# Kernel tuning notes

Hardware: AMD Instinct MI355X
Metric: run time of the kernel (lower is better)

The kernel has to match this reference:

```python
import jax, jax.numpy as jnp
import numpy as np

N = 10000   # nodes
E = 160000  # edges
D = 32      # hidden_dim == out_dim
IN = 2      # 'pos' node features
STEPS = 3   # GatedGraphConv n_steps


def setup_inputs() -> dict:
    key = jax.random.key(0)
    ks = jax.random.split(key, 16)
    s = 0.1  # init scale
    inp = {
        "x": jax.random.normal(ks[0], (N, IN), jnp.float32),
        "src": jax.random.randint(ks[1], (E,), 0, N, jnp.int64),
        "dst": jax.random.randint(ks[2], (E,), 0, N, jnp.int64),
        # node embedding Linear(in_dim, out_dim)
        "W_emb": jax.random.normal(ks[3], (IN, D), jnp.float32) * s,
        "b_emb": jnp.zeros((D,), jnp.float32),
        # EdgeConv: he = relu(theta(h_dst - h_src) + phi(h_src))
        "W_theta": jax.random.normal(ks[4], (D, D), jnp.float32) * s,
        "b_theta": jnp.zeros((D,), jnp.float32),
        "W_phi": jax.random.normal(ks[5], (D, D), jnp.float32) * s,
        "b_phi": jnp.zeros((D,), jnp.float32),
        # edge_func: Linear(D,64) -> ReLU -> Linear(64, D*D)
        "W1": jax.random.normal(ks[6], (D, 64), jnp.float32) * s,
        "b1": jnp.zeros((64,), jnp.float32),
        "W2": jax.random.normal(ks[7], (64, D * D), jnp.float32) * s,
        "b2": jnp.zeros((D * D,), jnp.float32),
        # GRUCell (torch convention), gates stacked [r|z|n]
        "W_ih": jax.random.normal(ks[8], (D, 3 * D), jnp.float32) * s,
        "b_ih": jnp.zeros((3 * D,), jnp.float32),
        "W_hh": jax.random.normal(ks[9], (D, 3 * D), jnp.float32) * s,
        "b_hh": jnp.zeros((3 * D,), jnp.float32),
    }
    return inp


def _gru_cell(a, h, W_ih, b_ih, W_hh, b_hh):
    gi = a @ W_ih + b_ih          # [N, 3D]
    gh = h @ W_hh + b_hh          # [N, 3D]
    i_r, i_z, i_n = jnp.split(gi, 3, axis=-1)
    h_r, h_z, h_n = jnp.split(gh, 3, axis=-1)
    r = jax.nn.sigmoid(i_r + h_r)
    z = jax.nn.sigmoid(i_z + h_z)
    n = jnp.tanh(i_n + r * h_n)
    return (1.0 - z) * n + z * h


def reference(x, src, dst, W_emb, b_emb, W_theta, b_theta, W_phi, b_phi,
              W1, b1, W2, b2, W_ih, b_ih, W_hh, b_hh):
    # node embedding
    h = x @ W_emb + b_emb                              # [N, D]
    # EdgeConv edge embedding (per edge)
    hs, hd = h[src], h[dst]                            # [E, D] gathers
    he = jax.nn.relu((hd - hs) @ W_theta + b_theta + hs @ W_phi + b_phi)  # [E, D]
    # NNConv-style per-edge weight matrices
    We = (jax.nn.relu(he @ W1 + b1) @ W2 + b2).reshape(E, D, D)           # [E, D, D]
    # gated (GRU) propagation for STEPS steps
    for _ in range(STEPS):
        msg = jnp.einsum('ei,eio->eo', h[src], We)     # per-edge gather-bmm
        a = jax.ops.segment_sum(msg, dst, num_segments=N)  # scatter-add [N, D]
        h = _gru_cell(a, h, W_ih, b_ih, W_hh, b_hh)
    return h
```

## Files before the change

### kernel.cpp

```cpp
#include <hip/hip_runtime.h>
#include <hip/hip_bf16.h>

#define D 32

typedef const float* fp;
typedef unsigned short u16;
typedef unsigned int u32;

using short8 = __attribute__((ext_vector_type(8))) short;
using f32x4  = __attribute__((ext_vector_type(4))) float;

__device__ __forceinline__ float b2f(u32 lo16) { return __uint_as_float(lo16 << 16); }
__device__ __forceinline__ u16 f2b(float f) {
    u32 x = __float_as_uint(f);
    return (u16)((x + 0x7fffu + ((x >> 16) & 1u)) >> 16);
}

__global__ void k_hev(fp x, fp W_emb, fp b_emb, fp Wth, fp bth, fp Wph, fp bph,
                      fp W2, u16* __restrict__ W2f, fp b2,
                      float* __restrict__ h, u16* __restrict__ hbf,
                      float* __restrict__ u, float* __restrict__ v,
                      float* __restrict__ B, float* __restrict__ a,
                      int* __restrict__ cnt, int* __restrict__ cursor,
                      int Npad, int N) {
    __shared__ float sP[192];
    __shared__ float shh[8][D];
    __shared__ float sb2[1024];
    int tid = threadIdx.x;
    if (tid < 32) {
        int o = tid;
        float au0 = 0.f, au1 = 0.f, cu = 0.f, av0 = 0.f, av1 = 0.f, cv = 0.f;
        for (int i = 0; i < D; ++i) {
            float wt = Wth[i * D + o];
            float wd = Wph[i * D + o] - wt;
            au0 += W_emb[i] * wt;
            au1 += W_emb[D + i] * wt;
            cu  += b_emb[i] * wt;
            av0 += W_emb[i] * wd;
            av1 += W_emb[D + i] * wd;
            cv  += b_emb[i] * wd;
        }
        sP[o]       = au0;
        sP[32 + o]  = au1;
        sP[64 + o]  = cu + bth[o] + bph[o];
        sP[96 + o]  = av0;
        sP[128 + o] = av1;
        sP[160 + o] = cv;
    }
    if (blockIdx.x < 256) {
        int idx = blockIdx.x * 256 + tid;
        int T = idx >> 9, r = idx & 511, l = r >> 3, j = r & 7;
        int ko = T * 16 + (l & 15);
        int i = (l >> 4) * 8 + j;
        W2f[idx] = f2b(W2[(size_t)(ko >> 5) * 1024 + i * 32 + (ko & 31)]);
    }
    for (int i = tid; i < 1024; i += 256) sb2[i] = b2[i];
    __syncthreads();
    int t = blockIdx.x * 256 + tid;
    bool active = (t < N * D);
    int n = t >> 5, o = t & 31;
    if (active) {
        a[t] = 0.f;
        if (t < Npad) cnt[t] = 0;
        if (t < N) cursor[t] = 0;
        float x0 = x[2 * n], x1 = x[2 * n + 1];
        float hv = x0 * W_emb[o] + x1 * W_emb[D + o] + b_emb[o];
        h[t] = hv;
        hbf[t] = f2b(hv);
        shh[tid >> 5][o] = hv;
        u[t] = x0 * sP[o] + x1 * sP[32 + o] + sP[64 + o];
        v[t] = x0 * sP[96 + o] + x1 * sP[128 + o] + sP[160 + o];
    }
    __syncthreads();
    if (active) {
        int lr = tid >> 5;
        float acc = 0.f;
        #pragma unroll 8
        for (int i = 0; i < D; ++i) acc += shh[lr][i] * sb2[i * 32 + o];
        B[t] = acc;
    }
}

__global__ void k_count(const int* __restrict__ src, int* __restrict__ cnt, int E) {
    int e = blockIdx.x * 256 + threadIdx.x;
    if (e < E) atomicAdd(&cnt[src[e]], 1);
}

__global__ void k_scan(const int* __restrict__ cnt, int* __restrict__ roff,
                       int* __restrict__ toff, int* __restrict__ tilS,
                       int* __restrict__ tilB, int N) {
    __shared__ int pe[1024], pt[1024];
    int t = threadIdx.x;
    int per = (N + 1023) / 1024;
    int begin = t * per, end = min(begin + per, N);
    int se = 0, st = 0;
    for (int i = begin; i < end; ++i) { int c = cnt[i]; se += c; st += (c + 15) >> 4; }
    pe[t] = se; pt[t] = st;
    __syncthreads();
    for (int off = 1; off < 1024; off <<= 1) {
        int ve = (t >= off) ? pe[t - off] : 0;
        int vt = (t >= off) ? pt[t - off] : 0;
        __syncthreads();
        pe[t] += ve; pt[t] += vt;
        __syncthreads();
    }
    int pre_e = (t == 0) ? 0 : pe[t - 1];
    int pre_t = (t == 0) ? 0 : pt[t - 1];
    for (int i = begin; i < end; ++i) {
        int c = cnt[i];
        roff[i] = pre_e;
        toff[i] = pre_t;
        int nt2 = (c + 15) >> 4;
        for (int q = 0; q < nt2; ++q) { tilS[pre_t + q] = i; tilB[pre_t + q] = pre_e + 16 * q; }
        pre_e += c;
        pre_t += nt2;
    }
    if (t == 0) { roff[N] = pe[1023]; toff[N] = pt[1023]; }
}

__global__ void k_scatter(const int* __restrict__ src, const int* __restrict__ dst,
                          const int* __restrict__ roff, int* __restrict__ cursor,
                          int* __restrict__ ssrc, int* __restrict__ sdst, int E) {
    int e = blockIdx.x * 256 + threadIdx.x;
    if (e >= E) return;
    int s = src[e];
    int p = roff[s] + atomicAdd(&cursor[s], 1);
    ssrc[p] = s;
    sdst[p] = dst[e];
}

__global__ __launch_bounds__(512)
void k_edge2(const float* __restrict__ u, const float* __restrict__ v,
             const int* __restrict__ ssrc, const int* __restrict__ sdst,
             fp W1, fp b1, u16* __restrict__ g, int E) {
    __shared__ float sW1[D * 64];
    __shared__ float sb1[64];
    __shared__ float she[8][2][D];
    for (int i = threadIdx.x; i < D * 64; i += 512) sW1[i] = W1[i];
    if (threadIdx.x < 64) sb1[threadIdx.x] = b1[threadIdx.x];
    __syncthreads();
    int w = threadIdx.x >> 6, lane = threadIdx.x & 63;
    int sub = lane >> 5, o = lane & 31;
    int gw = blockIdx.x * 8 + w;
    int stride = gridDim.x * 16;
    const float2* w2p = (const float2*)sW1;
    for (int e0 = gw * 2; e0 < E; e0 += stride) {
        int e = e0 + sub;
        bool val = (e < E);
        if (val) {
            int s = ssrc[e], d2 = sdst[e];
            she[w][sub][o] = fmaxf(u[(size_t)d2 * D + o] + v[(size_t)s * D + o], 0.f);
        }
        asm volatile("s_waitcnt lgkmcnt(0)" ::: "memory");
        __builtin_amdgcn_sched_barrier(0);
        if (val) {
            float a0 = sb1[2 * o], a1 = sb1[2 * o + 1];
            #pragma unroll
            for (int i = 0; i < D; ++i) {
                float hv = she[w][sub][i];
                float2 ww = w2p[i * 32 + o];
                a0 += hv * ww.x;
                a1 += hv * ww.y;
            }
            ((u32*)g)[(size_t)e * 32 + o] =
                (u32)f2b(fmaxf(a0, 0.f)) | ((u32)f2b(fmaxf(a1, 0.f)) << 16);
        }
        asm volatile("s_waitcnt lgkmcnt(0)" ::: "memory");
        __builtin_amdgcn_sched_barrier(0);
    }
}

__global__ __launch_bounds__(512)
void k_msgf(const u16* __restrict__ hbf, const u16* __restrict__ W2f,
            const float* __restrict__ Bv, const u32* __restrict__ g32,
            const int* __restrict__ tilS, const int* __restrict__ tilB,
            const int* __restrict__ roff, const int* __restrict__ toff,
            const int* __restrict__ sdst, float* __restrict__ a, int N) {
    __shared__ u32 sfrag[16 * 1024];
    int s0 = blockIdx.x * 16;
    int w = threadIdx.x >> 6, lp = threadIdx.x & 63;

    {
        int arow = s0 + (lp & 15);
        if (arow >= N) arow = N - 1;
        short8 afrag = *(const short8*)(hbf + (size_t)arow * 32 + (lp >> 4) * 8);
        int rbase = (lp >> 4) * 4;
        #pragma unroll
        for (int mi = 0; mi < 4; ++mi) {
            int k = w * 8 + 2 * mi;
            int kh = k >> 5;
            int kp = k & 31;
            int lt = ((kp >> 3) << 4) | (lp & 15);
            int jp = (kp & 7) >> 1;
            #pragma unroll
            for (int ot = 0; ot < 2; ++ot) {
                int T = 2 * k + ot;
                short8 bA = *(const short8*)(W2f + (size_t)T * 512 + lp * 8);
                short8 bB = *(const short8*)(W2f + (size_t)(T + 2) * 512 + lp * 8);
                f32x4 ca{0.f,0.f,0.f,0.f}, cb{0.f,0.f,0.f,0.f};
                ca = __builtin_amdgcn_mfma_f32_16x16x32_bf16(afrag, bA, ca, 0, 0, 0);
                cb = __builtin_amdgcn_mfma_f32_16x16x32_bf16(afrag, bB, cb, 0, 0, 0);
                int idx = (((kh << 1) | ot) << 8) + lt * 4 + jp;
                #pragma unroll
                for (int r = 0; r < 4; ++r)
                    sfrag[((rbase + r) << 10) + idx] =
                        (u32)f2b(ca[r]) | ((u32)f2b(cb[r]) << 16);
            }
        }
    }
    __syncthreads();

    int oc = lp & 15;
    int tbeg = toff[s0];
    int tend = toff[min(s0 + 16, N)];
    int ti = tbeg + w;
    uint4 A0c = make_uint4(0,0,0,0), A1c = A0c;
    int sC = 0, begC = 0, endC = 0;
    float Bs0c = 0.f, Bs1c = 0.f;
    if (ti < tend) {
        sC = tilS[ti]; begC = tilB[ti]; endC = roff[sC + 1];
        Bs0c = Bv[(size_t)sC * 32 + oc];
        Bs1c = Bv[(size_t)sC * 32 + 16 + oc];
        int er = begC + (lp & 15);
        if (er < endC) {
            const uint4* gp = (const uint4*)(g32 + (size_t)er * 32);
            A0c = gp[lp >> 4];
            A1c = gp[4 + (lp >> 4)];
        }
    }
    while (ti < tend) {
        int tn = ti + 8;
        uint4 A0n = make_uint4(0,0,0,0), A1n = A0n;
        int sN = 0, begN = 0, endN = 0;
        float Bs0n = 0.f, Bs1n = 0.f;
        if (tn < tend) {
            sN = tilS[tn]; begN = tilB[tn]; endN = roff[sN + 1];
            Bs0n = Bv[(size_t)sN * 32 + oc];
            Bs1n = Bv[(size_t)sN * 32 + 16 + oc];
            int er = begN + (lp & 15);
            if (er < endN) {
                const uint4* gp = (const uint4*)(g32 + (size_t)er * 32);
                A0n = gp[lp >> 4];
                A1n = gp[4 + (lp >> 4)];
            }
        }
        {
            union { uint4 u; short8 v; } A0, A1;
            A0.u = A0c; A1.u = A1c;
            const u32* mb = sfrag + ((sC - s0) << 10);
            union { uint4 u; short8 v; } B00, B01, B10, B11;
            B00.u = *(const uint4*)(mb + lp * 4);
            B01.u = *(const uint4*)(mb + 256 + lp * 4);
            B10.u = *(const uint4*)(mb + 512 + lp * 4);
            B11.u = *(const uint4*)(mb + 768 + lp * 4);
            f32x4 c0{0.f,0.f,0.f,0.f}, c1{0.f,0.f,0.f,0.f};
            __builtin_amdgcn_s_setprio(1);
            c0 = __builtin_amdgcn_mfma_f32_16x16x32_bf16(A0.v, B00.v, c0, 0, 0, 0);
            c0 = __builtin_amdgcn_mfma_f32_16x16x32_bf16(A1.v, B10.v, c0, 0, 0, 0);
            c1 = __builtin_amdgcn_mfma_f32_16x16x32_bf16(A0.v, B01.v, c1, 0, 0, 0);
            c1 = __builtin_amdgcn_mfma_f32_16x16x32_bf16(A1.v, B11.v, c1, 0, 0, 0);
            __builtin_amdgcn_s_setprio(0);
            int rb = (lp >> 4) * 4;
            #pragma unroll
            for (int r = 0; r < 4; ++r) {
                int e = begC + rb + r;
                if (e < endC) {
                    int d = sdst[e];
                    atomicAdd(&a[(size_t)d * 32 + oc],      c0[r] + Bs0c);
                    atomicAdd(&a[(size_t)d * 32 + 16 + oc], c1[r] + Bs1c);
                }
            }
        }
        ti = tn; sC = sN; begC = begN; endC = endN;
        A0c = A0n; A1c = A1n; Bs0c = Bs0n; Bs1c = Bs1n;
    }
}

__global__ __launch_bounds__(256)
void k_gru(float* __restrict__ a, const float* __restrict__ h,
           fp W_ih, fp b_ih, fp W_hh, fp b_hh, fp b2,
           float* __restrict__ hout, u16* __restrict__ hbf,
           float* __restrict__ Bout, int N) {
    __shared__ float sWi[D * 96], sWh[D * 96], sbi[96], sbh[96];
    __shared__ float sa[32][D], sh[32][D];
    __shared__ float sb2[1024];
    for (int i = threadIdx.x; i < D * 96; i += 256) { sWi[i] = W_ih[i]; sWh[i] = W_hh[i]; }
    for (int i = threadIdx.x; i < 1024; i += 256) sb2[i] = b2[i];
    if (threadIdx.x < 96) { sbi[threadIdx.x] = b_ih[threadIdx.x]; sbh[threadIdx.x] = b_hh[threadIdx.x]; }
    int n0 = blockIdx.x * 32;
    for (int i = threadIdx.x; i < 32 * D; i += 256) {
        int n = n0 + (i >> 5);
        if (n < N) {
            size_t idx = (size_t)n * D + (i & 31);
            sa[i >> 5][i & 31] = a[idx];
            sh[i >> 5][i & 31] = h[idx];
            a[idx] = 0.f;
        }
    }
    __syncthreads();
    int o = threadIdx.x & 31;
    #pragma unroll
    for (int z = 0; z < 4; ++z) {
        int sub = (threadIdx.x >> 5) + z * 8;
        int n = n0 + sub;
        if (n >= N) continue;
        float ir = sbi[o], iz = sbi[D + o], in_ = sbi[2 * D + o];
        float hr = sbh[o], hz = sbh[D + o], hn = sbh[2 * D + o];
        #pragma unroll
        for (int i = 0; i < D; ++i) {
            float av = sa[sub][i], hv = sh[sub][i];
            ir += av * sWi[i * 96 + o];
            iz += av * sWi[i * 96 + D + o];
            in_ += av * sWi[i * 96 + 2 * D + o];
            hr += hv * sWh[i * 96 + o];
            hz += hv * sWh[i * 96 + D + o];
            hn += hv * sWh[i * 96 + 2 * D + o];
        }
        float r = 1.f / (1.f + __expf(-(ir + hr)));
        float zz = 1.f / (1.f + __expf(-(iz + hz)));
        float nn = tanhf(in_ + r * hn);
        float hv2 = (1.f - zz) * nn + zz * sh[sub][o];
        size_t idx = (size_t)n * D + o;
        hout[idx] = hv2;
        hbf[idx] = f2b(hv2);
        sa[sub][o] = hv2;
    }
    __syncthreads();
    #pragma unroll
    for (int z = 0; z < 4; ++z) {
        int sub = (threadIdx.x >> 5) + z * 8;
        int n = n0 + sub;
        if (n >= N) continue;
        float acc = 0.f;
        #pragma unroll 8
        for (int i = 0; i < D; ++i) acc += sa[sub][i] * sb2[i * 32 + o];
        Bout[(size_t)n * D + o] = acc;
    }
}

extern "C" void kernel_launch(void* const* d_in, const int* in_sizes, int n_in,
                              void* d_out, int out_size, void* d_ws, size_t ws_size,
                              hipStream_t stream) {
    fp x      = (fp)d_in[0];
    const int* src = (const int*)d_in[1];
    const int* dst = (const int*)d_in[2];
    fp W_emb  = (fp)d_in[3];
    fp b_emb  = (fp)d_in[4];
    fp W_th   = (fp)d_in[5];
    fp b_th   = (fp)d_in[6];
    fp W_ph   = (fp)d_in[7];
    fp b_ph   = (fp)d_in[8];
    fp W1     = (fp)d_in[9];
    fp b1     = (fp)d_in[10];
    fp W2     = (fp)d_in[11];
    fp b2     = (fp)d_in[12];
    fp W_ih   = (fp)d_in[13];
    fp b_ih   = (fp)d_in[14];
    fp W_hh   = (fp)d_in[15];
    fp b_hh   = (fp)d_in[16];

    const int N = in_sizes[0] / 2;
    const int E = in_sizes[1];
    const int Npad = N + 4 - (N % 4);
    const int maxTiles = N + (E + 15) / 16;

    float* a      = (float*)d_ws;
    int*   cnt    = (int*)(a + (size_t)N * D);
    int*   cursor = cnt + Npad;
    int*   roff   = cursor + N;
    int*   toff   = roff + Npad;
    int*   ssrc   = toff + Npad;
    int*   sdst   = ssrc + E;
    int*   tilS   = sdst + E;
    int*   tilB   = tilS + maxTiles;
    float* hA     = (float*)(tilB + maxTiles);
    float* hB     = hA + (size_t)N * D;
    u16*   g      = (u16*)(hB + (size_t)N * D);
    u16*   hbf    = g + (size_t)E * 64;
    u16*   W2f    = hbf + (size_t)N * D;
    float* u      = (float*)(W2f + 65536);
    float* v      = u + (size_t)N * D;
    float* B      = v + (size_t)N * D;

    int ndBlocks = (N * D + 255) / 256;
    int eBlocks  = (E + 255) / 256;

    k_hev<<<ndBlocks, 256, 0, stream>>>(x, W_emb, b_emb, W_th, b_th, W_ph, b_ph,
                                        W2, W2f, b2, hA, hbf, u, v, B,
                                        a, cnt, cursor, Npad, N);
    k_count<<<eBlocks, 256, 0, stream>>>(src, cnt, E);
    k_scan<<<1, 1024, 0, stream>>>(cnt, roff, toff, tilS, tilB, N);
    k_scatter<<<eBlocks, 256, 0, stream>>>(src, dst, roff, cursor, ssrc, sdst, E);
    k_edge2<<<2048, 512, 0, stream>>>(u, v, ssrc, sdst, W1, b1, g, E);

    int fBlocks = (N + 15) / 16;
    float* hc = hA;
    float* hn_ = hB;
    for (int step = 0; step < 3; ++step) {
        k_msgf<<<fBlocks, 512, 0, stream>>>(hbf, W2f, B, (const u32*)g, tilS, tilB,
                                            roff, toff, sdst, a, N);
        float* dstbuf = (step == 2) ? (float*)d_out : hn_;
        k_gru<<<(N + 31) / 32, 256, 0, stream>>>(a, hc, W_ih, b_ih, W_hh, b_hh, b2,
                                                 dstbuf, hbf, B, N);
        float* t = hc; hc = hn_; hn_ = t;
    }
}
```

Measured before the change: 238.7 us.

## Replace atomic scatter-add with per-edge message buffer and CSR gather by destination

Instead of atomically adding each edge message into the node accumulator, the message kernel writes per-edge messages to a buffer, and the GRU kernel gathers them through a destination-sorted edge list built during preprocessing. This aims to remove float atomic contention and the zeroing of the accumulator. The cost is extra preprocessing (a second count, scan and scatter), plus an E×32 float buffer written and read back each step.

```diff
diff --git a/kernel.cpp b/kernel.cpp
--- a/kernel.cpp
+++ b/kernel.cpp
@@ -20,9 +20,7 @@
                       fp W2, u16* __restrict__ W2f, fp b2,
                       float* __restrict__ h, u16* __restrict__ hbf,
                       float* __restrict__ u, float* __restrict__ v,
-                      float* __restrict__ B, float* __restrict__ a,
-                      int* __restrict__ cnt, int* __restrict__ cursor,
-                      int Npad, int N) {
+                      float* __restrict__ B, int* __restrict__ zbase, int N) {
     __shared__ float sP[192];
     __shared__ float shh[8][D];
     __shared__ float sb2[1024];
@@ -60,9 +58,7 @@
     bool active = (t < N * D);
     int n = t >> 5, o = t & 31;
     if (active) {
-        a[t] = 0.f;
-        if (t < Npad) cnt[t] = 0;
-        if (t < N) cursor[t] = 0;
+        if (t < 4 * N) zbase[t] = 0;
         float x0 = x[2 * n], x1 = x[2 * n + 1];
         float hv = x0 * W_emb[o] + x1 * W_emb[D + o] + b_emb[o];
         h[t] = hv;
@@ -81,52 +77,64 @@
     }
 }
 
-__global__ void k_count(const int* __restrict__ src, int* __restrict__ cnt, int E) {
+__global__ void k_count(const int* __restrict__ src, const int* __restrict__ dst,
+                        int* __restrict__ cnt, int* __restrict__ cnt2, int E) {
     int e = blockIdx.x * 256 + threadIdx.x;
-    if (e < E) atomicAdd(&cnt[src[e]], 1);
-}
-
-__global__ void k_scan(const int* __restrict__ cnt, int* __restrict__ roff,
-                       int* __restrict__ toff, int* __restrict__ tilS,
+    if (e < E) { atomicAdd(&cnt[src[e]], 1); atomicAdd(&cnt2[dst[e]], 1); }
+}
+
+__global__ void k_scan(const int* __restrict__ cnt, const int* __restrict__ cnt2,
+                       int* __restrict__ roff, int* __restrict__ toff,
+                       int* __restrict__ doff, int* __restrict__ tilS,
                        int* __restrict__ tilB, int N) {
-    __shared__ int pe[1024], pt[1024];
+    __shared__ int pe[1024], pt[1024], pd[1024];
     int t = threadIdx.x;
     int per = (N + 1023) / 1024;
     int begin = t * per, end = min(begin + per, N);
-    int se = 0, st = 0;
-    for (int i = begin; i < end; ++i) { int c = cnt[i]; se += c; st += (c + 15) >> 4; }
-    pe[t] = se; pt[t] = st;
+    int se = 0, st = 0, sd = 0;
+    for (int i = begin; i < end; ++i) {
+        int c = cnt[i]; se += c; st += (c + 15) >> 4; sd += cnt2[i];
+    }
+    pe[t] = se; pt[t] = st; pd[t] = sd;
     __syncthreads();
     for (int off = 1; off < 1024; off <<= 1) {
         int ve = (t >= off) ? pe[t - off] : 0;
         int vt = (t >= off) ? pt[t - off] : 0;
+        int vd = (t >= off) ? pd[t - off] : 0;
         __syncthreads();
-        pe[t] += ve; pt[t] += vt;
+        pe[t] += ve; pt[t] += vt; pd[t] += vd;
         __syncthreads();
     }
     int pre_e = (t == 0) ? 0 : pe[t - 1];
     int pre_t = (t == 0) ? 0 : pt[t - 1];
+    int pre_d = (t == 0) ? 0 : pd[t - 1];
     for (int i = begin; i < end; ++i) {
         int c = cnt[i];
         roff[i] = pre_e;
         toff[i] = pre_t;
+        doff[i] = pre_d;
         int nt2 = (c + 15) >> 4;
         for (int q = 0; q < nt2; ++q) { tilS[pre_t + q] = i; tilB[pre_t + q] = pre_e + 16 * q; }
         pre_e += c;
         pre_t += nt2;
-    }
-    if (t == 0) { roff[N] = pe[1023]; toff[N] = pt[1023]; }
+        pre_d += cnt2[i];
+    }
+    if (t == 0) { roff[N] = pe[1023]; toff[N] = pt[1023]; doff[N] = pd[1023]; }
 }
 
 __global__ void k_scatter(const int* __restrict__ src, const int* __restrict__ dst,
-                          const int* __restrict__ roff, int* __restrict__ cursor,
-                          int* __restrict__ ssrc, int* __restrict__ sdst, int E) {
+                          const int* __restrict__ roff, const int* __restrict__ doff,
+                          int* __restrict__ cursor, int* __restrict__ cursor2,
+                          int* __restrict__ ssrc, int* __restrict__ sdst,
+                          int* __restrict__ elist, int E) {
     int e = blockIdx.x * 256 + threadIdx.x;
     if (e >= E) return;
-    int s = src[e];
+    int s = src[e], d = dst[e];
     int p = roff[s] + atomicAdd(&cursor[s], 1);
     ssrc[p] = s;
-    sdst[p] = dst[e];
+    sdst[p] = d;
+    int p2 = doff[d] + atomicAdd(&cursor2[d], 1);
+    elist[p2] = p;
 }
 
 __global__ __launch_bounds__(512)
@@ -175,7 +183,7 @@
             const float* __restrict__ Bv, const u32* __restrict__ g32,
             const int* __restrict__ tilS, const int* __restrict__ tilB,
             const int* __restrict__ roff, const int* __restrict__ toff,
-            const int* __restrict__ sdst, float* __restrict__ a, int N) {
+            float* __restrict__ msgbuf, int N) {
     __shared__ u32 sfrag[16 * 1024];
     int s0 = blockIdx.x * 16;
     int w = threadIdx.x >> 6, lp = threadIdx.x & 63;
@@ -265,9 +273,8 @@
             for (int r = 0; r < 4; ++r) {
                 int e = begC + rb + r;
                 if (e < endC) {
-                    int d = sdst[e];
-                    atomicAdd(&a[(size_t)d * 32 + oc],      c0[r] + Bs0c);
-                    atomicAdd(&a[(size_t)d * 32 + 16 + oc], c1[r] + Bs1c);
+                    msgbuf[(size_t)e * 32 + oc]      = c0[r] + Bs0c;
+                    msgbuf[(size_t)e * 32 + 16 + oc] = c1[r] + Bs1c;
                 }
             }
         }
@@ -277,31 +284,46 @@
 }
 
 __global__ __launch_bounds__(256)
-void k_gru(float* __restrict__ a, const float* __restrict__ h,
-           fp W_ih, fp b_ih, fp W_hh, fp b_hh, fp b2,
-           float* __restrict__ hout, u16* __restrict__ hbf,
-           float* __restrict__ Bout, int N) {
+void k_aggru(const float* __restrict__ msgbuf, const int* __restrict__ doff,
+             const int* __restrict__ elist, const float* __restrict__ h,
+             fp W_ih, fp b_ih, fp W_hh, fp b_hh, fp b2,
+             float* __restrict__ hout, u16* __restrict__ hbf,
+             float* __restrict__ Bout, int N) {
     __shared__ float sWi[D * 96], sWh[D * 96], sbi[96], sbh[96];
     __shared__ float sa[32][D], sh[32][D];
     __shared__ float sb2[1024];
+    __shared__ int sidx[8][8];
     for (int i = threadIdx.x; i < D * 96; i += 256) { sWi[i] = W_ih[i]; sWh[i] = W_hh[i]; }
     for (int i = threadIdx.x; i < 1024; i += 256) sb2[i] = b2[i];
     if (threadIdx.x < 96) { sbi[threadIdx.x] = b_ih[threadIdx.x]; sbh[threadIdx.x] = b_hh[threadIdx.x]; }
+    int hw = threadIdx.x >> 5, o = threadIdx.x & 31;
     int n0 = blockIdx.x * 32;
-    for (int i = threadIdx.x; i < 32 * D; i += 256) {
-        int n = n0 + (i >> 5);
-        if (n < N) {
-            size_t idx = (size_t)n * D + (i & 31);
-            sa[i >> 5][i & 31] = a[idx];
-            sh[i >> 5][i & 31] = h[idx];
-            a[idx] = 0.f;
-        }
-    }
-    __syncthreads();
-    int o = threadIdx.x & 31;
     #pragma unroll
     for (int z = 0; z < 4; ++z) {
-        int sub = (threadIdx.x >> 5) + z * 8;
+        int sub = hw + z * 8;
+        int d = n0 + sub;
+        float acc = 0.f;
+        if (d < N) {
+            int b = doff[d], e2 = doff[d + 1];
+            for (int c0 = b; c0 < e2; c0 += 8) {
+                if (o < 8 && c0 + o < e2) sidx[hw][o] = elist[c0 + o];
+                asm volatile("s_waitcnt lgkmcnt(0)" ::: "memory");
+                __builtin_amdgcn_sched_barrier(0);
+                float m[8];
+                #pragma unroll
+                for (int j = 0; j < 8; ++j)
+                    m[j] = (c0 + j < e2) ? msgbuf[(size_t)sidx[hw][j] * 32 + o] : 0.f;
+                #pragma unroll
+                for (int j = 0; j < 8; ++j) acc += m[j];
+            }
+            sh[sub][o] = h[(size_t)d * D + o];
+        }
+        sa[sub][o] = acc;
+    }
+    __syncthreads();
+    #pragma unroll
+    for (int z = 0; z < 4; ++z) {
+        int sub = hw + z * 8;
         int n = n0 + sub;
         if (n >= N) continue;
         float ir = sbi[o], iz = sbi[D + o], in_ = sbi[2 * D + o];
@@ -328,7 +350,7 @@
     __syncthreads();
     #pragma unroll
     for (int z = 0; z < 4; ++z) {
-        int sub = (threadIdx.x >> 5) + z * 8;
+        int sub = hw + z * 8;
         int n = n0 + sub;
         if (n >= N) continue;
         float acc = 0.f;
@@ -361,17 +383,21 @@
 
     const int N = in_sizes[0] / 2;
     const int E = in_sizes[1];
-    const int Npad = N + 4 - (N % 4);
+    const int Np1 = ((N + 1 + 3) / 4) * 4;
     const int maxTiles = N + (E + 15) / 16;
 
-    float* a      = (float*)d_ws;
-    int*   cnt    = (int*)(a + (size_t)N * D);
-    int*   cursor = cnt + Npad;
-    int*   roff   = cursor + N;
-    int*   toff   = roff + Npad;
-    int*   ssrc   = toff + Npad;
+    float* msgbuf = (float*)d_ws;
+    int*   cnt    = (int*)(msgbuf + (size_t)E * 32);
+    int*   cursor = cnt + N;
+    int*   cnt2   = cursor + N;
+    int*   cursor2= cnt2 + N;
+    int*   roff   = cursor2 + N;
+    int*   toff   = roff + Np1;
+    int*   doff   = toff + Np1;
+    int*   ssrc   = doff + Np1;
     int*   sdst   = ssrc + E;
-    int*   tilS   = sdst + E;
+    int*   elist  = sdst + E;
+    int*   tilS   = elist + E;
     int*   tilB   = tilS + maxTiles;
     float* hA     = (float*)(tilB + maxTiles);
     float* hB     = hA + (size_t)N * D;
@@ -386,11 +412,11 @@
     int eBlocks  = (E + 255) / 256;
 
     k_hev<<<ndBlocks, 256, 0, stream>>>(x, W_emb, b_emb, W_th, b_th, W_ph, b_ph,
-                                        W2, W2f, b2, hA, hbf, u, v, B,
-                                        a, cnt, cursor, Npad, N);
-    k_count<<<eBlocks, 256, 0, stream>>>(src, cnt, E);
-    k_scan<<<1, 1024, 0, stream>>>(cnt, roff, toff, tilS, tilB, N);
-    k_scatter<<<eBlocks, 256, 0, stream>>>(src, dst, roff, cursor, ssrc, sdst, E);
+                                        W2, W2f, b2, hA, hbf, u, v, B, cnt, N);
+    k_count<<<eBlocks, 256, 0, stream>>>(src, dst, cnt, cnt2, E);
+    k_scan<<<1, 1024, 0, stream>>>(cnt, cnt2, roff, toff, doff, tilS, tilB, N);
+    k_scatter<<<eBlocks, 256, 0, stream>>>(src, dst, roff, doff, cursor, cursor2,
+                                           ssrc, sdst, elist, E);
     k_edge2<<<2048, 512, 0, stream>>>(u, v, ssrc, sdst, W1, b1, g, E);
 
     int fBlocks = (N + 15) / 16;
@@ -398,10 +424,11 @@
     float* hn_ = hB;
     for (int step = 0; step < 3; ++step) {
         k_msgf<<<fBlocks, 512, 0, stream>>>(hbf, W2f, B, (const u32*)g, tilS, tilB,
-                                            roff, toff, sdst, a, N);
+                                            roff, toff, msgbuf, N);
         float* dstbuf = (step == 2) ? (float*)d_out : hn_;
-        k_gru<<<(N + 31) / 32, 256, 0, stream>>>(a, hc, W_ih, b_ih, W_hh, b_hh, b2,
-                                                 dstbuf, hbf, B, N);
+        k_aggru<<<(N + 31) / 32, 256, 0, stream>>>(msgbuf, doff, elist, hc,
+                                                   W_ih, b_ih, W_hh, b_hh, b2,
+                                                   dstbuf, hbf, B, N);
         float* t = hc; hc = hn_; hn_ = t;
     }
 }
```

Result: slower. 253.3 us (+6.1%).
